# Optimization experiments

Hardware: AMD Instinct MI355X
Metric: run time of the kernel (lower is better)

## Reference

```python
import jax, jax.numpy as jnp
import numpy as np

N_DATA = 40000   # max_training_points
D_PCA = 16       # n_pca_components
D_FEAT = 384     # raw feature dim
Q = 8192         # number of query points


def setup_inputs() -> dict:
    key = jax.random.key(0)
    k1, k2, k3, k4, k5 = jax.random.split(key, 5)
    features = jax.random.normal(k1, (Q, D_FEAT), dtype=jnp.float32)
    pca_mean = jax.random.normal(k2, (D_FEAT,), dtype=jnp.float32) * 0.1
    singular_vectors = jax.random.normal(k3, (D_FEAT, D_PCA), dtype=jnp.float32) / np.sqrt(D_FEAT)
    max_length = jnp.asarray(4.0, dtype=jnp.float32)  # max L2 norm seen at fit time
    # bw_transform is lower-triangular (Cholesky of scaled inverse covariance)
    bw = jax.random.normal(k4, (D_PCA, D_PCA), dtype=jnp.float32) * 0.2
    bw_transform = jnp.tril(bw) + 1.5 * jnp.eye(D_PCA, dtype=jnp.float32)
    dataset = jax.random.normal(k5, (N_DATA, D_PCA), dtype=jnp.float32)  # already bw-transformed at fit
    # norm = prod(diag(bw)) * (2*pi)^(-d/2)
    norm = jnp.prod(jnp.diag(bw_transform)) * jnp.asarray((2 * np.pi) ** (-D_PCA / 2), jnp.float32)
    return {
        'features': features,
        'pca_mean': pca_mean,
        'singular_vectors': singular_vectors,
        'max_length': max_length,
        'bw_transform': bw_transform,
        'dataset': dataset,
        'norm': norm,
    }


def reference(features, pca_mean, singular_vectors, max_length, bw_transform, dataset, norm):
    # PCA.transform: center then project
    f = jnp.matmul(features - pca_mean, singular_vectors)          # [Q, d]
    # pre_process with SCALE method
    f = f / max_length
    # GaussianKDE.forward: bandwidth transform then pairwise sq-dist to dataset
    f = jnp.matmul(f, bw_transform)                                # [Q, d]
    # ||dataset_j - f_i||^2 = |f|^2 + |ds|^2 - 2 f.ds  (vectorized, no QxNxd tensor)
    d2 = (jnp.sum(f * f, axis=1, keepdims=True)
          + jnp.sum(dataset * dataset, axis=1)[None, :]
          - 2.0 * jnp.matmul(f, dataset.T))                        # [Q, N]
    estimate = jnp.mean(jnp.exp(-0.5 * d2), axis=1) * norm         # [Q]
    scores = jnp.log(estimate + 1e-300)                            # log-likelihood
    # compute_probabilities
    return 1.0 / (1.0 + jnp.exp(0.05 * (scores - 12.0)))
```

## Files before the change

### kernel.cpp

```cpp
#include <hip/hip_runtime.h>
#include <hip/hip_bf16.h>

#define Q 8192
#define DF 384
#define DP 16
#define NDATA 40000
#define AUGK 32
#define QPRE_BLOCKS 512
#define DPRE_BLOCKS ((NDATA + 255) / 256)
#define NQBLK 64
#define QB_PER_BLK 128
#define SCH_C 126.95703125f
#define P23 8388608.f

typedef __attribute__((ext_vector_type(8))) short short8v;
typedef __attribute__((ext_vector_type(4))) float f32x4;

__device__ __forceinline__ unsigned short f2bf(float x) {
    union { float f; unsigned int u; } c; c.f = x;
    unsigned int u = c.u;
    u += 0x7fff + ((u >> 16) & 1);
    return (unsigned short)(u >> 16);
}
__device__ __forceinline__ float bf2f(unsigned short h) {
    union { float f; unsigned int u; } c; c.u = ((unsigned int)h) << 16;
    return c.f;
}
__device__ __forceinline__ float i2f_bits(int i) {
    union { int i; float f; } c; c.i = i; return c.f;
}
__device__ __forceinline__ float fexp2(float x) {
#if __has_builtin(__builtin_amdgcn_exp2f)
    return __builtin_amdgcn_exp2f(x);
#else
    float r; asm volatile("v_exp_f32 %0, %1" : "=v"(r) : "v"(x)); return r;
#endif
}

__global__ __launch_bounds__(384) void k_mm(
    const float* __restrict__ mean, const float* __restrict__ sv,
    const float* __restrict__ bw, const float* __restrict__ maxlen_p,
    float* __restrict__ M2, float* __restrict__ cc)
{
    __shared__ float bwl[256];
    __shared__ float red[384];
    __shared__ float cmps[16];
    int t = threadIdx.x;
    if (t < 256) bwl[t] = bw[t];
    {
        int k = t & 15, s = t >> 4;
        float a = 0.f;
        for (int d = s; d < DF; d += 24)
            a = fmaf(mean[d], sv[d * DP + k], a);
        red[t] = a;
    }
    __syncthreads();
    float scale = P23 * 1.4426950408889634f / (*maxlen_p);
    {
        const float4* s4 = (const float4*)(sv + (size_t)t * DP);
        float4 a0 = s4[0], a1 = s4[1], a2 = s4[2], a3 = s4[3];
        float svr[16] = {a0.x, a0.y, a0.z, a0.w, a1.x, a1.y, a1.z, a1.w,
                         a2.x, a2.y, a2.z, a2.w, a3.x, a3.y, a3.z, a3.w};
        float mrow[16];
#pragma unroll
        for (int j = 0; j < 16; ++j) {
            float m = 0.f;
#pragma unroll
            for (int k = 0; k < 16; ++k) m = fmaf(svr[k], bwl[k * 16 + j], m);
            mrow[j] = scale * m;
        }
        float4* md = (float4*)(M2 + (size_t)t * DP);
        md[0] = make_float4(mrow[0], mrow[1], mrow[2], mrow[3]);
        md[1] = make_float4(mrow[4], mrow[5], mrow[6], mrow[7]);
        md[2] = make_float4(mrow[8], mrow[9], mrow[10], mrow[11]);
        md[3] = make_float4(mrow[12], mrow[13], mrow[14], mrow[15]);
    }
    if (t < 16) {
        float m = 0.f;
        for (int s = 0; s < 24; ++s) m += red[s * 16 + t];
        cmps[t] = m;
    }
    __syncthreads();
    if (t < 16) {
        float s = 0.f;
#pragma unroll
        for (int k = 0; k < 16; ++k) s = fmaf(cmps[k], bwl[k * 16 + t], s);
        cc[t] = scale * s;
    }
}

__global__ __launch_bounds__(256) void k_pre(
    const float* __restrict__ feat, const float* __restrict__ ds,
    const float* __restrict__ M2, const float* __restrict__ cc,
    unsigned short* __restrict__ cfb, float* __restrict__ qb,
    unsigned short* __restrict__ dsb)
{
    int t = threadIdx.x;

    if (blockIdx.x >= QPRE_BLOCKS) {
        int j = (int)(blockIdx.x - QPRE_BLOCKS) * 256 + t;
        if (j < NDATA) {
            const float4* r = (const float4*)(ds + (size_t)j * DP);
            unsigned int pk[8];
            float ss = 0.f;
#pragma unroll
            for (int q4 = 0; q4 < 4; ++q4) {
                float4 v = r[q4];
                unsigned short h0 = f2bf(v.x), h1 = f2bf(v.y);
                unsigned short h2 = f2bf(v.z), h3 = f2bf(v.w);
                float f0 = bf2f(h0), f1 = bf2f(h1), f2 = bf2f(h2), f3 = bf2f(h3);
                ss += f0 * f0 + f1 * f1 + f2 * f2 + f3 * f3;
                pk[q4 * 2 + 0] = (unsigned int)h0 | ((unsigned int)h1 << 16);
                pk[q4 * 2 + 1] = (unsigned int)h2 | ((unsigned int)h3 << 16);
            }
            float v = fmaf(ss, -0.72134752044f, SCH_C);
            unsigned short hi = f2bf(v);
            unsigned short lo = f2bf(v - bf2f(hi));
            uint4* dst = (uint4*)(dsb + (size_t)j * AUGK);
            dst[0] = make_uint4(pk[0], pk[1], pk[2], pk[3]);
            dst[1] = make_uint4(pk[4], pk[5], pk[6], pk[7]);
            dst[2] = make_uint4((unsigned int)hi | ((unsigned int)lo << 16), 0u, 0u, 0u);
            dst[3] = make_uint4(0u, 0u, 0u, 0u);
        }
        return;
    }

    __shared__ __align__(16) float m2l[DF * 20];
    __shared__ float ccl[16];
    const float4* m2g = (const float4*)M2;
#pragma unroll
    for (int it = 0; it < 6; ++it) {
        int i = it * 256 + t;
        int d = i >> 2, qq = i & 3;
        *(float4*)(m2l + d * 20 + qq * 4) = m2g[i];
    }
    if (t < 16) ccl[t] = cc[t];
    __syncthreads();

    int r = t >> 4, s = t & 15;
    int row = (int)blockIdx.x * 16 + r;
    float acc[16];
#pragma unroll
    for (int k = 0; k < 16; ++k) acc[k] = 0.f;
    const float* fr = feat + (size_t)row * DF;
#pragma unroll 4
    for (int c = 0; c < 24; ++c) {
        int d = s + (c << 4);
        float fv = fr[d];
        const float4* mr = (const float4*)(m2l + d * 20);
        float4 m0 = mr[0], m1 = mr[1], m2 = mr[2], m3 = mr[3];
        acc[0]  = fmaf(fv, m0.x, acc[0]);  acc[1]  = fmaf(fv, m0.y, acc[1]);
        acc[2]  = fmaf(fv, m0.z, acc[2]);  acc[3]  = fmaf(fv, m0.w, acc[3]);
        acc[4]  = fmaf(fv, m1.x, acc[4]);  acc[5]  = fmaf(fv, m1.y, acc[5]);
        acc[6]  = fmaf(fv, m1.z, acc[6]);  acc[7]  = fmaf(fv, m1.w, acc[7]);
        acc[8]  = fmaf(fv, m2.x, acc[8]);  acc[9]  = fmaf(fv, m2.y, acc[9]);
        acc[10] = fmaf(fv, m2.z, acc[10]); acc[11] = fmaf(fv, m2.w, acc[11]);
        acc[12] = fmaf(fv, m3.x, acc[12]); acc[13] = fmaf(fv, m3.y, acc[13]);
        acc[14] = fmaf(fv, m3.z, acc[14]); acc[15] = fmaf(fv, m3.w, acc[15]);
    }
#pragma unroll
    for (int k = 0; k < 16; ++k) {
        acc[k] += __shfl_xor(acc[k], 1);
        acc[k] += __shfl_xor(acc[k], 2);
        acc[k] += __shfl_xor(acc[k], 4);
        acc[k] += __shfl_xor(acc[k], 8);
    }
    if (s == 0) {
        unsigned int pk[16];
        unsigned short h[16];
        float s2 = 0.f;
#pragma unroll
        for (int k = 0; k < 16; ++k) {
            float f = acc[k] - ccl[k];
            h[k] = f2bf(f);
            float fr2 = bf2f(h[k]) * (1.f / P23);
            s2 += fr2 * fr2;
        }
        qb[row] = -0.34657359028f * s2;
#pragma unroll
        for (int p = 0; p < 8; ++p)
            pk[p] = (unsigned int)h[2 * p] | ((unsigned int)h[2 * p + 1] << 16);
        pk[8] = 0x4B004B00u;
#pragma unroll
        for (int p = 9; p < 16; ++p) pk[p] = 0u;
        uint4* dst = (uint4*)(cfb + (size_t)row * AUGK);
        dst[0] = make_uint4(pk[0], pk[1], pk[2], pk[3]);
        dst[1] = make_uint4(pk[4], pk[5], pk[6], pk[7]);
        dst[2] = make_uint4(pk[8], pk[9], pk[10], pk[11]);
        dst[3] = make_uint4(pk[12], pk[13], pk[14], pk[15]);
    }
}

__global__ __launch_bounds__(256) void k3_main(
    const unsigned short* __restrict__ cfb, const unsigned short* __restrict__ dsb,
    float* __restrict__ partial, int cs)
{
    int qblk = (int)blockIdx.x % NQBLK;
    int c    = (int)blockIdx.x / NQBLK;
    int w = threadIdx.x >> 6, l = threadIdx.x & 63;
    int qbase = qblk * QB_PER_BLK + w * 32;
    int kg = l >> 4, col = l & 15;

    const short8v* ap = (const short8v*)(cfb + (size_t)(qbase + col) * AUGK + kg * 8);
    short8v a0 = ap[0];
    short8v a1 = ap[64];

    int j0 = c * cs;
    int j1 = min(NDATA, j0 + cs);
    int ntile = (j1 - j0) >> 4;

    const short8v* bp = (const short8v*)(dsb + (size_t)(j0 + col) * AUGK + kg * 8);

    float sacc[2][4] = {{0.f, 0.f, 0.f, 0.f}, {0.f, 0.f, 0.f, 0.f}};
    f32x4 z = {0.f, 0.f, 0.f, 0.f};

#pragma unroll 4
    for (int it = 0; it < ntile; ++it) {
        short8v bf = bp[(size_t)it * 64];
        f32x4 d0 = __builtin_amdgcn_mfma_f32_16x16x32_bf16(a0, bf, z, 0, 0, 0);
        f32x4 d1 = __builtin_amdgcn_mfma_f32_16x16x32_bf16(a1, bf, z, 0, 0, 0);
#pragma unroll
        for (int r = 0; r < 4; ++r) {
            sacc[0][r] += i2f_bits((int)d0[r]);
            sacc[1][r] += i2f_bits((int)d1[r]);
        }
    }

#pragma unroll
    for (int o = 1; o < 16; o <<= 1)
#pragma unroll
        for (int tt = 0; tt < 2; ++tt)
#pragma unroll
            for (int r = 0; r < 4; ++r)
                sacc[tt][r] += __shfl_xor(sacc[tt][r], o);

    if (col == 0) {
        float* dst = partial + (size_t)c * Q + qbase;
#pragma unroll
        for (int tt = 0; tt < 2; ++tt)
#pragma unroll
            for (int r = 0; r < 4; ++r)
                dst[tt * 16 + kg * 4 + r] = sacc[tt][r];
    }
}

__global__ __launch_bounds__(256) void k4_final(
    const float* __restrict__ partial, const float* __restrict__ qb,
    const float* __restrict__ norm_p, float* __restrict__ out, int nd)
{
    __shared__ float l2[8][33];
    int t = threadIdx.x;
    int ql = t & 31, sl = t >> 5;
    int q = (int)blockIdx.x * 32 + ql;
    float a = 0.f;
    for (int cc = sl; cc < nd; cc += 8) a += partial[(size_t)cc * Q + q];
    l2[sl][ql] = a;
    __syncthreads();
    if (t < 32) {
        int qq = (int)blockIdx.x * 32 + t;
        float s = 0.f;
#pragma unroll
        for (int s8 = 0; s8 < 8; ++s8) s += l2[s8][t];
        float est = (*norm_p) * (1.0f / (float)NDATA) * fexp2(qb[qq]) * s;
        float score = logf(est + 1e-38f);
        out[qq] = 1.0f / (1.0f + expf(0.05f * (score - 12.0f)));
    }
}

extern "C" void kernel_launch(void* const* d_in, const int* in_sizes, int n_in,
                              void* d_out, int out_size, void* d_ws, size_t ws_size,
                              hipStream_t stream) {
    const float* features = (const float*)d_in[0];
    const float* pca_mean = (const float*)d_in[1];
    const float* sv       = (const float*)d_in[2];
    const float* maxlen   = (const float*)d_in[3];
    const float* bw       = (const float*)d_in[4];
    const float* dataset  = (const float*)d_in[5];
    const float* norm     = (const float*)d_in[6];
    float* out = (float*)d_out;

    char* ws = (char*)d_ws;
    unsigned short* cfb = (unsigned short*)(ws);
    unsigned short* dsb = (unsigned short*)(ws + 524288);
    float* qb = (float*)(ws + 524288 + 2560000);
    float* M2 = (float*)(ws + 524288 + 2560000 + 32768);
    float* cc = (float*)(ws + 524288 + 2560000 + 32768 + 24576);
    float* partial = (float*)(ws + 524288 + 2560000 + 32768 + 24576 + 256);
    size_t head = 524288 + 2560000 + 32768 + 24576 + 256;

    int nd = 32;
    size_t avail = (ws_size > head) ? (ws_size - head) / ((size_t)Q * 4) : 1;
    if ((size_t)nd > avail) nd = (int)avail;
    if (nd < 1) nd = 1;
    int tiles = NDATA / 16;
    int tpc = (tiles + nd - 1) / nd;
    int cs = tpc * 16;
    nd = (tiles + tpc - 1) / tpc;

    k_mm<<<1, 384, 0, stream>>>(pca_mean, sv, bw, maxlen, M2, cc);
    k_pre<<<QPRE_BLOCKS + DPRE_BLOCKS, 256, 0, stream>>>(
        features, dataset, M2, cc, cfb, qb, dsb);
    k3_main<<<NQBLK * nd, 256, 0, stream>>>(cfb, dsb, partial, cs);
    k4_final<<<Q / 32, 256, 0, stream>>>(partial, qb, norm, out, nd);
}
```

Baseline: 128.0 us.

## Fuse final reduction into main kernel via atomics and last-block epilogue

The main MFMA kernel now covers 64 queries per wave (four A fragments) so each loaded dataset tile is reused across more queries. It also splits the dataset into many more chunks (40 tiles each). Per-chunk sums go to a global estimate array with atomicAdd, and the last block per query group, found through an atomic counter, computes the final probabilities. This removes the separate final kernel and the partial buffer, at the cost of a memset, float atomic contention and a non-deterministic summation order.

Result: slower. 243.3 us (+90.0%).

```diff
diff --git a/kernel.cpp b/kernel.cpp
--- a/kernel.cpp
+++ b/kernel.cpp
@@ -8,8 +8,7 @@
 #define AUGK 32
 #define QPRE_BLOCKS 512
 #define DPRE_BLOCKS ((NDATA + 255) / 256)
-#define NQBLK 64
-#define QB_PER_BLK 128
+#define NQBLK3 32
 #define SCH_C 126.95703125f
 #define P23 8388608.f
 
@@ -191,19 +190,26 @@
     }
 }
 
-__global__ __launch_bounds__(256) void k3_main(
+__global__ __launch_bounds__(256, 8) void k3_main(
     const unsigned short* __restrict__ cfb, const unsigned short* __restrict__ dsb,
-    float* __restrict__ partial, int cs)
+    const float* __restrict__ qb, const float* __restrict__ norm_p,
+    float* __restrict__ est, int* __restrict__ cnt,
+    float* __restrict__ out, int cs, int nd)
 {
-    int qblk = (int)blockIdx.x % NQBLK;
-    int c    = (int)blockIdx.x / NQBLK;
-    int w = threadIdx.x >> 6, l = threadIdx.x & 63;
-    int qbase = qblk * QB_PER_BLK + w * 32;
+    __shared__ float est_l[256];
+    __shared__ int lastf;
+    int t = threadIdx.x;
+    int qblk = (int)blockIdx.x % NQBLK3;
+    int c    = (int)blockIdx.x / NQBLK3;
+    int w = t >> 6, l = t & 63;
+    int qbase = qblk * 256 + w * 64;
     int kg = l >> 4, col = l & 15;
 
     const short8v* ap = (const short8v*)(cfb + (size_t)(qbase + col) * AUGK + kg * 8);
     short8v a0 = ap[0];
     short8v a1 = ap[64];
+    short8v a2 = ap[128];
+    short8v a3 = ap[192];
 
     int j0 = c * cs;
     int j1 = min(NDATA, j0 + cs);
@@ -211,59 +217,54 @@
 
     const short8v* bp = (const short8v*)(dsb + (size_t)(j0 + col) * AUGK + kg * 8);
 
-    float sacc[2][4] = {{0.f, 0.f, 0.f, 0.f}, {0.f, 0.f, 0.f, 0.f}};
+    float sacc[4][4] = {{0.f,0.f,0.f,0.f},{0.f,0.f,0.f,0.f},
+                        {0.f,0.f,0.f,0.f},{0.f,0.f,0.f,0.f}};
     f32x4 z = {0.f, 0.f, 0.f, 0.f};
 
-#pragma unroll 4
     for (int it = 0; it < ntile; ++it) {
         short8v bf = bp[(size_t)it * 64];
         f32x4 d0 = __builtin_amdgcn_mfma_f32_16x16x32_bf16(a0, bf, z, 0, 0, 0);
         f32x4 d1 = __builtin_amdgcn_mfma_f32_16x16x32_bf16(a1, bf, z, 0, 0, 0);
+        f32x4 d2 = __builtin_amdgcn_mfma_f32_16x16x32_bf16(a2, bf, z, 0, 0, 0);
+        f32x4 d3 = __builtin_amdgcn_mfma_f32_16x16x32_bf16(a3, bf, z, 0, 0, 0);
 #pragma unroll
         for (int r = 0; r < 4; ++r) {
             sacc[0][r] += i2f_bits((int)d0[r]);
             sacc[1][r] += i2f_bits((int)d1[r]);
+            sacc[2][r] += i2f_bits((int)d2[r]);
+            sacc[3][r] += i2f_bits((int)d3[r]);
         }
     }
 
 #pragma unroll
     for (int o = 1; o < 16; o <<= 1)
 #pragma unroll
-        for (int tt = 0; tt < 2; ++tt)
+        for (int tt = 0; tt < 4; ++tt)
 #pragma unroll
             for (int r = 0; r < 4; ++r)
                 sacc[tt][r] += __shfl_xor(sacc[tt][r], o);
 
     if (col == 0) {
-        float* dst = partial + (size_t)c * Q + qbase;
-#pragma unroll
-        for (int tt = 0; tt < 2; ++tt)
+#pragma unroll
+        for (int tt = 0; tt < 4; ++tt)
 #pragma unroll
             for (int r = 0; r < 4; ++r)
-                dst[tt * 16 + kg * 4 + r] = sacc[tt][r];
-    }
-}
-
-__global__ __launch_bounds__(256) void k4_final(
-    const float* __restrict__ partial, const float* __restrict__ qb,
-    const float* __restrict__ norm_p, float* __restrict__ out, int nd)
-{
-    __shared__ float l2[8][33];
-    int t = threadIdx.x;
-    int ql = t & 31, sl = t >> 5;
-    int q = (int)blockIdx.x * 32 + ql;
-    float a = 0.f;
-    for (int cc = sl; cc < nd; cc += 8) a += partial[(size_t)cc * Q + q];
-    l2[sl][ql] = a;
-    __syncthreads();
-    if (t < 32) {
-        int qq = (int)blockIdx.x * 32 + t;
-        float s = 0.f;
-#pragma unroll
-        for (int s8 = 0; s8 < 8; ++s8) s += l2[s8][t];
-        float est = (*norm_p) * (1.0f / (float)NDATA) * fexp2(qb[qq]) * s;
-        float score = logf(est + 1e-38f);
-        out[qq] = 1.0f / (1.0f + expf(0.05f * (score - 12.0f)));
+                est_l[w * 64 + tt * 16 + kg * 4 + r] = sacc[tt][r];
+    }
+    __syncthreads();
+
+    atomicAdd(&est[qblk * 256 + t], est_l[t]);
+    __threadfence();
+    __syncthreads();
+    if (t == 0) lastf = (atomicAdd(&cnt[qblk], 1) == nd - 1) ? 1 : 0;
+    __syncthreads();
+
+    if (lastf) {
+        int q = qblk * 256 + t;
+        float s = atomicAdd(&est[q], 0.0f);
+        float ev = (*norm_p) * (1.0f / (float)NDATA) * fexp2(qb[q]) * s;
+        float score = logf(ev + 1e-38f);
+        out[q] = 1.0f / (1.0f + expf(0.05f * (score - 12.0f)));
     }
 }
 
@@ -280,26 +281,22 @@
     float* out = (float*)d_out;
 
     char* ws = (char*)d_ws;
-    unsigned short* cfb = (unsigned short*)(ws);
-    unsigned short* dsb = (unsigned short*)(ws + 524288);
-    float* qb = (float*)(ws + 524288 + 2560000);
-    float* M2 = (float*)(ws + 524288 + 2560000 + 32768);
-    float* cc = (float*)(ws + 524288 + 2560000 + 32768 + 24576);
-    float* partial = (float*)(ws + 524288 + 2560000 + 32768 + 24576 + 256);
-    size_t head = 524288 + 2560000 + 32768 + 24576 + 256;
-
-    int nd = 32;
-    size_t avail = (ws_size > head) ? (ws_size - head) / ((size_t)Q * 4) : 1;
-    if ((size_t)nd > avail) nd = (int)avail;
-    if (nd < 1) nd = 1;
+    float* est = (float*)ws;
+    int* cnt = (int*)(ws + 32768);
+    unsigned short* cfb = (unsigned short*)(ws + 33024);
+    unsigned short* dsb = (unsigned short*)(ws + 33024 + 524288);
+    float* qb = (float*)(ws + 33024 + 524288 + 2560000);
+    float* M2 = (float*)(ws + 33024 + 524288 + 2560000 + 32768);
+    float* cc = (float*)(ws + 33024 + 524288 + 2560000 + 32768 + 24576);
+
     int tiles = NDATA / 16;
-    int tpc = (tiles + nd - 1) / nd;
+    int tpc = 40;
     int cs = tpc * 16;
-    nd = (tiles + tpc - 1) / tpc;
-
+    int nd = (tiles + tpc - 1) / tpc;
+
+    hipMemsetAsync(est, 0, 33024, stream);
     k_mm<<<1, 384, 0, stream>>>(pca_mean, sv, bw, maxlen, M2, cc);
     k_pre<<<QPRE_BLOCKS + DPRE_BLOCKS, 256, 0, stream>>>(
         features, dataset, M2, cc, cfb, qb, dsb);
-    k3_main<<<NQBLK * nd, 256, 0, stream>>>(cfb, dsb, partial, cs);
-    k4_final<<<Q / 32, 256, 0, stream>>>(partial, qb, norm, out, nd);
-}
+    k3_main<<<NQBLK3 * nd, 256, 0, stream>>>(cfb, dsb, qb, norm, est, cnt, out, cs, nd);
+}
```

## Widen per-wave query tile, double-buffer dataset loads, fix 64-chunk split

Applied to the files above, without the earlier changes.

Each wave now covers 64 queries (four MFMA A-fragments) instead of 32, so every dataset fragment loaded is reused across twice as many MFMAs. The main loop is software-pipelined with a two-tile prefetch of dataset fragments, and the dataset is split into a fixed 64 balanced chunks across 2048 blocks, with an occupancy hint of 8 blocks per CU. The cost is more accumulator registers per thread, and the removal of the workspace-size check: the kernel now assumes the workspace holds 64 partial-sum rows.

After: 118.2 us (median of 2 runs). 1.08x faster.

```diff
diff --git a/kernel.cpp b/kernel.cpp
--- a/kernel.cpp
+++ b/kernel.cpp
@@ -8,8 +8,8 @@
 #define AUGK 32
 #define QPRE_BLOCKS 512
 #define DPRE_BLOCKS ((NDATA + 255) / 256)
-#define NQBLK 64
-#define QB_PER_BLK 128
+#define NQBLK3 32
+#define NCHUNK 64
 #define SCH_C 126.95703125f
 #define P23 8388608.f
 
@@ -191,45 +191,69 @@
     }
 }
 
-__global__ __launch_bounds__(256) void k3_main(
+#define COMPT(bf)                                                             \
+    {                                                                         \
+        f32x4 d0 = __builtin_amdgcn_mfma_f32_16x16x32_bf16(a0, bf, z, 0, 0, 0); \
+        f32x4 d1 = __builtin_amdgcn_mfma_f32_16x16x32_bf16(a1, bf, z, 0, 0, 0); \
+        f32x4 d2 = __builtin_amdgcn_mfma_f32_16x16x32_bf16(a2, bf, z, 0, 0, 0); \
+        f32x4 d3 = __builtin_amdgcn_mfma_f32_16x16x32_bf16(a3, bf, z, 0, 0, 0); \
+        _Pragma("unroll")                                                     \
+        for (int r = 0; r < 4; ++r) {                                         \
+            sacc[0][r] += i2f_bits((int)d0[r]);                               \
+            sacc[1][r] += i2f_bits((int)d1[r]);                               \
+            sacc[2][r] += i2f_bits((int)d2[r]);                               \
+            sacc[3][r] += i2f_bits((int)d3[r]);                               \
+        }                                                                     \
+    }
+
+__global__ __launch_bounds__(256, 8) void k3_main(
     const unsigned short* __restrict__ cfb, const unsigned short* __restrict__ dsb,
-    float* __restrict__ partial, int cs)
+    float* __restrict__ partial)
 {
-    int qblk = (int)blockIdx.x % NQBLK;
-    int c    = (int)blockIdx.x / NQBLK;
-    int w = threadIdx.x >> 6, l = threadIdx.x & 63;
-    int qbase = qblk * QB_PER_BLK + w * 32;
+    int t = threadIdx.x;
+    int qblk = (int)blockIdx.x & (NQBLK3 - 1);
+    int c    = (int)blockIdx.x >> 5;
+    int w = t >> 6, l = t & 63;
+    int qbase = qblk * 256 + w * 64;
     int kg = l >> 4, col = l & 15;
+
+    int start = c * 39 + min(c, 4);
+    int ntile = 39 + (c < 4 ? 1 : 0);
+    int j0 = start * 16;
 
     const short8v* ap = (const short8v*)(cfb + (size_t)(qbase + col) * AUGK + kg * 8);
     short8v a0 = ap[0];
     short8v a1 = ap[64];
-
-    int j0 = c * cs;
-    int j1 = min(NDATA, j0 + cs);
-    int ntile = (j1 - j0) >> 4;
+    short8v a2 = ap[128];
+    short8v a3 = ap[192];
 
     const short8v* bp = (const short8v*)(dsb + (size_t)(j0 + col) * AUGK + kg * 8);
 
-    float sacc[2][4] = {{0.f, 0.f, 0.f, 0.f}, {0.f, 0.f, 0.f, 0.f}};
+    float sacc[4][4] = {{0.f,0.f,0.f,0.f},{0.f,0.f,0.f,0.f},
+                        {0.f,0.f,0.f,0.f},{0.f,0.f,0.f,0.f}};
     f32x4 z = {0.f, 0.f, 0.f, 0.f};
 
-#pragma unroll 4
-    for (int it = 0; it < ntile; ++it) {
-        short8v bf = bp[(size_t)it * 64];
-        f32x4 d0 = __builtin_amdgcn_mfma_f32_16x16x32_bf16(a0, bf, z, 0, 0, 0);
-        f32x4 d1 = __builtin_amdgcn_mfma_f32_16x16x32_bf16(a1, bf, z, 0, 0, 0);
-#pragma unroll
-        for (int r = 0; r < 4; ++r) {
-            sacc[0][r] += i2f_bits((int)d0[r]);
-            sacc[1][r] += i2f_bits((int)d1[r]);
-        }
+    int npair = ntile >> 1;
+    short8v bf0 = bp[0];
+    short8v bf1 = bp[64];
+    for (int p = 0; p + 1 < npair; ++p) {
+        short8v n0 = bp[(size_t)(2 * p + 2) * 64];
+        short8v n1 = bp[(size_t)(2 * p + 3) * 64];
+        COMPT(bf0);
+        COMPT(bf1);
+        bf0 = n0; bf1 = n1;
+    }
+    COMPT(bf0);
+    COMPT(bf1);
+    if (ntile & 1) {
+        short8v bl = bp[(size_t)(ntile - 1) * 64];
+        COMPT(bl);
     }
 
 #pragma unroll
     for (int o = 1; o < 16; o <<= 1)
 #pragma unroll
-        for (int tt = 0; tt < 2; ++tt)
+        for (int tt = 0; tt < 4; ++tt)
 #pragma unroll
             for (int r = 0; r < 4; ++r)
                 sacc[tt][r] += __shfl_xor(sacc[tt][r], o);
@@ -237,7 +261,7 @@
     if (col == 0) {
         float* dst = partial + (size_t)c * Q + qbase;
 #pragma unroll
-        for (int tt = 0; tt < 2; ++tt)
+        for (int tt = 0; tt < 4; ++tt)
 #pragma unroll
             for (int r = 0; r < 4; ++r)
                 dst[tt * 16 + kg * 4 + r] = sacc[tt][r];
@@ -246,14 +270,14 @@
 
 __global__ __launch_bounds__(256) void k4_final(
     const float* __restrict__ partial, const float* __restrict__ qb,
-    const float* __restrict__ norm_p, float* __restrict__ out, int nd)
+    const float* __restrict__ norm_p, float* __restrict__ out)
 {
     __shared__ float l2[8][33];
     int t = threadIdx.x;
     int ql = t & 31, sl = t >> 5;
     int q = (int)blockIdx.x * 32 + ql;
     float a = 0.f;
-    for (int cc = sl; cc < nd; cc += 8) a += partial[(size_t)cc * Q + q];
+    for (int cc = sl; cc < NCHUNK; cc += 8) a += partial[(size_t)cc * Q + q];
     l2[sl][ql] = a;
     __syncthreads();
     if (t < 32) {
@@ -286,20 +310,10 @@
     float* M2 = (float*)(ws + 524288 + 2560000 + 32768);
     float* cc = (float*)(ws + 524288 + 2560000 + 32768 + 24576);
     float* partial = (float*)(ws + 524288 + 2560000 + 32768 + 24576 + 256);
-    size_t head = 524288 + 2560000 + 32768 + 24576 + 256;
-
-    int nd = 32;
-    size_t avail = (ws_size > head) ? (ws_size - head) / ((size_t)Q * 4) : 1;
-    if ((size_t)nd > avail) nd = (int)avail;
-    if (nd < 1) nd = 1;
-    int tiles = NDATA / 16;
-    int tpc = (tiles + nd - 1) / nd;
-    int cs = tpc * 16;
-    nd = (tiles + tpc - 1) / tpc;
 
     k_mm<<<1, 384, 0, stream>>>(pca_mean, sv, bw, maxlen, M2, cc);
     k_pre<<<QPRE_BLOCKS + DPRE_BLOCKS, 256, 0, stream>>>(
         features, dataset, M2, cc, cfb, qb, dsb);
-    k3_main<<<NQBLK * nd, 256, 0, stream>>>(cfb, dsb, partial, cs);
-    k4_final<<<Q / 32, 256, 0, stream>>>(partial, qb, norm, out, nd);
-}
+    k3_main<<<NQBLK3 * NCHUNK, 256, 0, stream>>>(cfb, dsb, partial);
+    k4_final<<<Q / 32, 256, 0, stream>>>(partial, qb, norm, out);
+}
```
